# Kernel tuning notes

Measured on AMD Instinct MI355X. Metric: run time of the kernel, lower is better.

Reference implementation:

```python
import jax, jax.numpy as jnp
import numpy as np
import math

BN_EPS = 1e-5
L2_EPS = 1e-12
TEMPARATURE = 0.01
Q_IN_DIM = 256


def _masked_bn(y, mask, gamma, beta):
    # y: [S, L, D], mask: [S, L] float (1 = valid packed row).
    # Emulates BatchNorm1d (training mode) over the packed valid rows.
    m = mask[..., None]
    cnt = jnp.sum(mask)
    mean = jnp.sum(y * m, axis=(0, 1)) / cnt
    var = jnp.sum(jnp.square(y - mean) * m, axis=(0, 1)) / cnt  # biased var
    return (y - mean) * jax.lax.rsqrt(var + BN_EPS) * gamma + beta


def _ctx_proj(x, W, b, gamma, beta, mask, normalize):
    y = jnp.einsum('sld,od->slo', x, W) + b
    y = jax.nn.relu(_masked_bn(y, mask, gamma, beta))
    if normalize:
        n = jnp.linalg.norm(y, axis=-1, keepdims=True)
        y = y / jnp.maximum(n, L2_EPS)
    return y


def setup_inputs() -> dict:
    key = jax.random.key(0)
    ks = jax.random.split(key, 8)
    S, La, Lb = 256, 128, 512
    Dq, Dkv, Dqk, Dv = 256, 265, 512, 512
    A = jax.random.normal(ks[0], (S, La, Dq), jnp.float32)
    B = jax.random.normal(ks[1], (S, Lb, Dkv), jnp.float32)
    a_lens = jax.random.randint(ks[2], (S,), 1, La + 1, jnp.int32)
    b_lens = jax.random.randint(ks[3], (S,), 1, Lb + 1, jnp.int32)
    pk = jax.random.split(ks[4], 4)
    sc = 0.05
    return {
        'A': A, 'B': B, 'a_lens': a_lens, 'b_lens': b_lens,
        'Wq': sc * jax.random.normal(pk[0], (Dqk, Dq), jnp.float32),
        'bq': jnp.zeros((Dqk,), jnp.float32),
        'gq': jnp.ones((Dqk,), jnp.float32),
        'betaq': jnp.zeros((Dqk,), jnp.float32),
        'Wk': sc * jax.random.normal(pk[1], (Dqk, Dkv), jnp.float32),
        'bk': jnp.zeros((Dqk,), jnp.float32),
        'gk': jnp.ones((Dqk,), jnp.float32),
        'betak': jnp.zeros((Dqk,), jnp.float32),
        'Wv': sc * jax.random.normal(pk[2], (Dv, Dkv), jnp.float32),
        'bv': jnp.zeros((Dv,), jnp.float32),
        'gv': jnp.ones((Dv,), jnp.float32),
        'betav': jnp.zeros((Dv,), jnp.float32),
        'Wf': sc * jax.random.normal(pk[3], (Dq, Dv), jnp.float32),
        'bf': jnp.zeros((Dq,), jnp.float32),
        'gf': jnp.ones((Dq,), jnp.float32),
        'betaf': jnp.zeros((Dq,), jnp.float32),
    }


def reference(A, B, a_lens, b_lens,
              Wq, bq, gq, betaq,
              Wk, bk, gk, betak,
              Wv, bv, gv, betav,
              Wf, bf, gf, betaf):
    S, La, _ = A.shape
    Lb = B.shape[1]
    mask_a = (jnp.arange(La)[None, :] < a_lens[:, None]).astype(A.dtype)  # [S, La]
    mask_b = (jnp.arange(Lb)[None, :] < b_lens[:, None]).astype(B.dtype)  # [S, Lb]

    q = _ctx_proj(A, Wq, bq, gq, betaq, mask_a, True)   # [S, La, Dqk]
    k = _ctx_proj(B, Wk, bk, gk, betak, mask_b, True)   # [S, Lb, Dqk]
    v = _ctx_proj(B, Wv, bv, gv, betav, mask_b, True)   # [S, Lb, Dv]

    scaler = 1.0 / (TEMPARATURE * math.sqrt(Q_IN_DIM))
    scores = jnp.einsum('sad,sbd->sab', q, k) * scaler  # [S, La, Lb]
    scores = jnp.where(mask_b[:, None, :] > 0, scores, -1e30)
    w = jax.nn.softmax(scores, axis=-1)
    wv = jnp.einsum('sab,sbd->sad', w, v)               # [S, La, Dv]

    f = _ctx_proj(wv, Wf, bf, gf, betaf, mask_a, False)  # [S, La, Dq]
    return f * mask_a[..., None]
```

## Files before the change

### kernel.cpp

```cpp
#include <hip/hip_runtime.h>
#include <hip/hip_bf16.h>
#include <stdint.h>


typedef __attribute__((ext_vector_type(8))) short short8;
typedef __attribute__((ext_vector_type(4))) float floatx4;

__device__ __forceinline__ float bf2f(short h) {
    union { unsigned u; float f; } c;
    c.u = ((unsigned)(unsigned short)h) << 16;
    return c.f;
}
__device__ __forceinline__ short f2bf(float f) {
    union { float f; unsigned u; } c;
    c.f = f;
    unsigned u = c.u + 0x7fffu + ((c.u >> 16) & 1u);
    return (short)(u >> 16);
}

__device__ __forceinline__ void async_cp16(const short* g, short* l) {
    __builtin_amdgcn_global_load_lds(
        (const __attribute__((address_space(1))) unsigned int*)g,
        (__attribute__((address_space(3))) unsigned int*)l, 16, 0, 0);
}

__device__ __forceinline__ short8 cvt8load(const float* p) {
    float4 f0 = *(const float4*)(p);
    float4 f1 = *(const float4*)(p + 4);
    short8 r;
    r[0] = f2bf(f0.x); r[1] = f2bf(f0.y); r[2] = f2bf(f0.z); r[3] = f2bf(f0.w);
    r[4] = f2bf(f1.x); r[5] = f2bf(f1.y); r[6] = f2bf(f1.z); r[7] = f2bf(f1.w);
    return r;
}
__device__ __forceinline__ short8 cvt8guard(const float* row, int c0, int Kin) {
    short8 r;
#pragma unroll
    for (int j = 0; j < 8; j++) {
        int c = c0 + j;
        r[j] = (c < Kin) ? f2bf(row[c]) : (short)0;
    }
    return r;
}

__global__ __launch_bounds__(256) void cvt_pad(const float* __restrict__ in,
                                               short* __restrict__ out,
                                               int kin, int kout) {
    long row = blockIdx.x;
    const float* src = in + row * (long)kin;
    short* dst = out + row * (long)kout;
    for (int c = threadIdx.x; c < kout; c += 256)
        dst[c] = (c < kin) ? f2bf(src[c]) : (short)0;
}

__global__ __launch_bounds__(256, 2)
void gemm128x2(const short* __restrict__ X,
               const short* __restrict__ W0, const short* __restrict__ W1,
               const float* __restrict__ bias0, const float* __restrict__ bias1,
               short* __restrict__ Y0, short* __restrict__ Y1,
               float* __restrict__ st0, float* __restrict__ st1,
               int N, int Kp, const int* __restrict__ lens, int Lshift,
               int nShift)
{
    __shared__ short SH[36864];
    const int lin = blockIdx.x;
    const int xcd = lin & 7, sl = lin >> 3;
    const int nb = sl & ((1 << nShift) - 1);
    const int ms = sl >> nShift;
    const int m0 = (ms * 8 + xcd) * 128;
    const int n0 = nb * 128;

    const int tid = threadIdx.x;
    const int l = tid & 63, w = tid >> 6;
    const int quad = l >> 4, l15 = l & 15;
    const int wr = w & 1, wc = w >> 1;
    const int mo = wr * 64, no = wc * 64;

    floatx4 acc0[4][4], acc1[4][4];
#pragma unroll
    for (int i = 0; i < 4; i++)
#pragma unroll
        for (int j = 0; j < 4; j++) {
            acc0[i][j] = (floatx4){0.f, 0.f, 0.f, 0.f};
            acc1[i][j] = (floatx4){0.f, 0.f, 0.f, 0.f};
        }

    int srow[2], scolS[2];
#pragma unroll
    for (int c = 0; c < 2; c++) {
        int L = tid * 16 + c * 4096;
        int S = L ^ ((((L >> 6) ^ (L >> 8)) & 1) << 4)
                  ^ (((L >> 7) & 1) << 5)
                  ^ (((L >> 8) & 1) << 6);
        srow[c] = S >> 6;
        scolS[c] = (S & 48) >> 1;
    }
    const short* Xs[2];
    const short* W0s[2];
    const short* W1s[2];
#pragma unroll
    for (int c = 0; c < 2; c++) {
        Xs[c]  = X  + (long)(m0 + srow[c]) * Kp + scolS[c];
        W0s[c] = W0 + (long)(n0 + srow[c]) * Kp + scolS[c];
        W1s[c] = W1 + (long)(n0 + srow[c]) * Kp + scolS[c];
    }
    const int nsteps = Kp >> 5;

    int rsA[4], rsB[4];
#pragma unroll
    for (int i = 0; i < 4; i++) {
        int rA = mo + i * 16 + l15;
        int rB = no + i * 16 + l15;
        rsA[i] = (rA << 6) ^ ((rA & 7) << 4) ^ (quad << 4);
        rsB[i] = (rB << 6) ^ ((rB & 7) << 4) ^ (quad << 4);
    }

    auto stage = [&](int buf, int t) {
        short* At = SH + buf * 12288;
        short* B0t = At + 4096;
        short* B1t = At + 8192;
        const int ko = t * 32;
#pragma unroll
        for (int c = 0; c < 2; c++)
            async_cp16(Xs[c] + ko, At + c * 2048 + tid * 8);
#pragma unroll
        for (int c = 0; c < 2; c++)
            async_cp16(W0s[c] + ko, B0t + c * 2048 + tid * 8);
#pragma unroll
        for (int c = 0; c < 2; c++)
            async_cp16(W1s[c] + ko, B1t + c * 2048 + tid * 8);
    };

    stage(0, 0);
    if (nsteps > 1) stage(1, 1);
    if (nsteps > 2) stage(2, 2);

    int cur = 0;
    for (int t = 0; t < nsteps; t++) {
        if (t + 2 < nsteps)      asm volatile("s_waitcnt vmcnt(12)" ::: "memory");
        else if (t + 1 < nsteps) asm volatile("s_waitcnt vmcnt(6)" ::: "memory");
        else                     asm volatile("s_waitcnt vmcnt(0)" ::: "memory");
        __builtin_amdgcn_s_barrier();
        __builtin_amdgcn_sched_barrier(0);

        const char* At = (const char*)(SH + cur * 12288);
        const char* B0t = At + 8192;
        const char* B1t = At + 16384;
        short8 af[4], bfr[4];
#pragma unroll
        for (int i = 0; i < 4; i++)
            af[i] = *(const short8*)(At + rsA[i]);
#pragma unroll
        for (int j = 0; j < 4; j++)
            bfr[j] = *(const short8*)(B0t + rsB[j]);
#pragma unroll
        for (int i = 0; i < 4; i++)
#pragma unroll
            for (int j = 0; j < 4; j++)
                acc0[i][j] = __builtin_amdgcn_mfma_f32_16x16x32_bf16(af[i], bfr[j], acc0[i][j], 0, 0, 0);
#pragma unroll
        for (int j = 0; j < 4; j++)
            bfr[j] = *(const short8*)(B1t + rsB[j]);
#pragma unroll
        for (int i = 0; i < 4; i++)
#pragma unroll
            for (int j = 0; j < 4; j++)
                acc1[i][j] = __builtin_amdgcn_mfma_f32_16x16x32_bf16(af[i], bfr[j], acc1[i][j], 0, 0, 0);

        __builtin_amdgcn_sched_barrier(0);
        __builtin_amdgcn_s_barrier();
        if (t + 3 < nsteps) stage(cur, t + 3);
        cur = (cur == 2) ? 0 : cur + 1;
    }

    const int Lmask = (1 << Lshift) - 1;
    float msk[4][4];
#pragma unroll
    for (int i = 0; i < 4; i++)
#pragma unroll
        for (int r = 0; r < 4; r++) {
            int rg = m0 + mo + i * 16 + quad * 4 + r;
            msk[i][r] = ((rg & Lmask) < lens[rg >> Lshift]) ? 1.f : 0.f;
        }
    short* Cs = SH;

    auto epi = [&](floatx4 (&acc)[4][4], const float* bias, float* stats, short* Y) {
        float bv[4];
#pragma unroll
        for (int j = 0; j < 4; j++) bv[j] = bias[n0 + no + j * 16 + l15];
#pragma unroll
        for (int j = 0; j < 4; j++) {
            float ps = 0.f, pss = 0.f;
#pragma unroll
            for (int i = 0; i < 4; i++)
#pragma unroll
                for (int r = 0; r < 4; r++) {
                    float v = acc[i][j][r] + bv[j];
                    ps += v * msk[i][r];
                    pss += v * v * msk[i][r];
                }
            ps  += __shfl_xor(ps, 16, 64);  ps  += __shfl_xor(ps, 32, 64);
            pss += __shfl_xor(pss, 16, 64); pss += __shfl_xor(pss, 32, 64);
            if (l < 16) {
                atomicAdd(&stats[n0 + no + j * 16 + l15], ps);
                atomicAdd(&stats[N + n0 + no + j * 16 + l15], pss);
            }
        }
#pragma unroll
        for (int pass = 0; pass < 2; pass++) {
            __syncthreads();
            if (wr == pass) {
#pragma unroll
                for (int j = 0; j < 4; j++)
#pragma unroll
                    for (int i = 0; i < 4; i++)
#pragma unroll
                        for (int r = 0; r < 4; r++)
                            Cs[(i * 16 + quad * 4 + r) * 132 + no + j * 16 + l15] =
                                f2bf(acc[i][j][r] + bv[j]);
            }
            __syncthreads();
#pragma unroll
            for (int c = 0; c < 4; c++) {
                int e = c * 2048 + tid * 8;
                int row = e >> 7, col = e & 127;
                short8 vv = *(const short8*)(Cs + row * 132 + col);
                *(short8*)(Y + (long)(m0 + pass * 64 + row) * N + n0 + col) = vv;
            }
        }
    };
    epi(acc0, bias0, st0, Y0);
    epi(acc1, bias1, st1, Y1);
}

__global__ __launch_bounds__(256, 3)
void gemm128(const short* __restrict__ X,
             const short* __restrict__ W0, const short* __restrict__ W1,
             const float* __restrict__ bias0, const float* __restrict__ bias1,
             short* __restrict__ Y0, short* __restrict__ Y1,
             float* __restrict__ st0, float* __restrict__ st1,
             int N, int Kp, const int* __restrict__ lens, int Lshift,
             int nShift, int dual)
{
    __shared__ short SH[24576];
    const int lin = blockIdx.x;
    const int xcd = lin & 7, sl = lin >> 3;
    const int nb = sl & ((1 << nShift) - 1);
    const int ms = sl >> nShift;
    const int m0 = (ms * 8 + xcd) * 128;
    int g = 0, n0;
    if (dual) { g = nb & 1; n0 = (nb >> 1) * 128; } else { n0 = nb * 128; }
    const short* W    = g ? W1 : W0;
    const float* bias = g ? bias1 : bias0;
    short* Y          = g ? Y1 : Y0;
    float* stats      = g ? st1 : st0;

    const int tid = threadIdx.x;
    const int l = tid & 63, w = tid >> 6;
    const int quad = l >> 4, l15 = l & 15;
    const int wr = w & 1, wc = w >> 1;
    const int mo = wr * 64, no = wc * 64;

    floatx4 acc[4][4];
#pragma unroll
    for (int i = 0; i < 4; i++)
#pragma unroll
        for (int j = 0; j < 4; j++) acc[i][j] = (floatx4){0.f, 0.f, 0.f, 0.f};

    const int srow = tid >> 2;
    const int scol = (tid & 3) * 8;
    const short* Xs = X + (long)(m0 + srow) * Kp + scol;
    const short* Ws = W + (long)(n0 + srow) * Kp + scol;
    const long strideR = (long)64 * Kp;
    const int nsteps = Kp >> 5;

    auto stage = [&](int buf, int t) {
        short* At = SH + buf * 8192;
        short* Bt = At + 4096;
        const short* Xk = Xs + t * 32;
        const short* Wk = Ws + t * 32;
        async_cp16(Xk,           At + tid * 8);
        async_cp16(Xk + strideR, At + 2048 + tid * 8);
        async_cp16(Wk,           Bt + tid * 8);
        async_cp16(Wk + strideR, Bt + 2048 + tid * 8);
    };

    stage(0, 0);
    if (nsteps > 1) stage(1, 1);
    if (nsteps > 2) stage(2, 2);

    int cur = 0;
    for (int t = 0; t < nsteps; t++) {
        if (t + 2 < nsteps)      asm volatile("s_waitcnt vmcnt(8)" ::: "memory");
        else if (t + 1 < nsteps) asm volatile("s_waitcnt vmcnt(4)" ::: "memory");
        else                     asm volatile("s_waitcnt vmcnt(0)" ::: "memory");
        __builtin_amdgcn_s_barrier();
        __builtin_amdgcn_sched_barrier(0);

        const short* At = SH + cur * 8192;
        const short* Bt = At + 4096;
        short8 af[4], bfr[4];
#pragma unroll
        for (int i = 0; i < 4; i++)
            af[i] = *(const short8*)(At + (mo + i * 16 + l15) * 32 + quad * 8);
#pragma unroll
        for (int j = 0; j < 4; j++)
            bfr[j] = *(const short8*)(Bt + (no + j * 16 + l15) * 32 + quad * 8);
#pragma unroll
        for (int i = 0; i < 4; i++)
#pragma unroll
            for (int j = 0; j < 4; j++)
                acc[i][j] = __builtin_amdgcn_mfma_f32_16x16x32_bf16(af[i], bfr[j], acc[i][j], 0, 0, 0);

        __builtin_amdgcn_sched_barrier(0);
        __builtin_amdgcn_s_barrier();
        if (t + 3 < nsteps) stage(cur, t + 3);
        cur = (cur == 2) ? 0 : cur + 1;
    }

    const int Lmask = (1 << Lshift) - 1;
    float msk[4][4];
#pragma unroll
    for (int i = 0; i < 4; i++)
#pragma unroll
        for (int r = 0; r < 4; r++) {
            int rg = m0 + mo + i * 16 + quad * 4 + r;
            msk[i][r] = ((rg & Lmask) < lens[rg >> Lshift]) ? 1.f : 0.f;
        }
    float bv[4];
#pragma unroll
    for (int j = 0; j < 4; j++) bv[j] = bias[n0 + no + j * 16 + l15];

#pragma unroll
    for (int j = 0; j < 4; j++) {
        float ps = 0.f, pss = 0.f;
#pragma unroll
        for (int i = 0; i < 4; i++)
#pragma unroll
            for (int r = 0; r < 4; r++) {
                float v = acc[i][j][r] + bv[j];
                ps += v * msk[i][r];
                pss += v * v * msk[i][r];
            }
        ps  += __shfl_xor(ps, 16, 64);  ps  += __shfl_xor(ps, 32, 64);
        pss += __shfl_xor(pss, 16, 64); pss += __shfl_xor(pss, 32, 64);
        if (l < 16) {
            atomicAdd(&stats[n0 + no + j * 16 + l15], ps);
            atomicAdd(&stats[N + n0 + no + j * 16 + l15], pss);
        }
    }

    short* Cs = SH;
#pragma unroll
    for (int pass = 0; pass < 2; pass++) {
        __syncthreads();
        if (wr == pass) {
#pragma unroll
            for (int j = 0; j < 4; j++)
#pragma unroll
                for (int i = 0; i < 4; i++)
#pragma unroll
                    for (int r = 0; r < 4; r++)
                        Cs[(i * 16 + quad * 4 + r) * 132 + no + j * 16 + l15] =
                            f2bf(acc[i][j][r] + bv[j]);
        }
        __syncthreads();
#pragma unroll
        for (int c = 0; c < 4; c++) {
            int e = c * 2048 + tid * 8;
            int row = e >> 7, col = e & 127;
            short8 vv = *(const short8*)(Cs + row * 132 + col);
            *(short8*)(Y + (long)(m0 + pass * 64 + row) * N + n0 + col) = vv;
        }
    }
}

template<bool XBF16, bool KAL>
__global__ __launch_bounds__(256, 2)
void gemm_bt(const void* __restrict__ Xp, const float* __restrict__ W,
             const float* __restrict__ bias, short* __restrict__ Y,
             int N, int Kin, int Kp, float* __restrict__ stats,
             const int* __restrict__ lens, int Lshift)
{
    __shared__ short At[128 * 32];
    __shared__ short Bt[128 * 32];
    const int m0 = blockIdx.x * 128;
    const int n0 = blockIdx.y * 128;
    const int tid = threadIdx.x;
    const int w = tid >> 6, l = tid & 63;
    const int quad = l >> 4, l15 = l & 15;
    const int mo = (w & 1) * 64, no = (w >> 1) * 64;

    floatx4 acc[4][4];
#pragma unroll
    for (int i = 0; i < 4; i++)
#pragma unroll
        for (int j = 0; j < 4; j++) acc[i][j] = (floatx4){0.f, 0.f, 0.f, 0.f};

    const int srow = tid >> 2;
    const int sc8 = (tid & 3) * 8;

    for (int k0 = 0; k0 < Kp; k0 += 32) {
        __syncthreads();
        const int c0 = k0 + sc8;
        short8 a0, a1, b0, b1;
        if (XBF16) {
            const short* X = (const short*)Xp;
            a0 = *(const short8*)(X + (long)(m0 + srow) * Kp + c0);
            a1 = *(const short8*)(X + (long)(m0 + 64 + srow) * Kp + c0);
        } else {
            const float* X = (const float*)Xp;
            if (KAL) {
                a0 = cvt8load(X + (long)(m0 + srow) * Kin + c0);
                a1 = cvt8load(X + (long)(m0 + 64 + srow) * Kin + c0);
            } else {
                a0 = cvt8guard(X + (long)(m0 + srow) * Kin, c0, Kin);
                a1 = cvt8guard(X + (long)(m0 + 64 + srow) * Kin, c0, Kin);
            }
        }
        if (KAL) {
            b0 = cvt8load(W + (long)(n0 + srow) * Kin + c0);
            b1 = cvt8load(W + (long)(n0 + 64 + srow) * Kin + c0);
        } else {
            b0 = cvt8guard(W + (long)(n0 + srow) * Kin, c0, Kin);
            b1 = cvt8guard(W + (long)(n0 + 64 + srow) * Kin, c0, Kin);
        }
        *(short8*)(At + srow * 32 + sc8) = a0;
        *(short8*)(At + (64 + srow) * 32 + sc8) = a1;
        *(short8*)(Bt + srow * 32 + sc8) = b0;
        *(short8*)(Bt + (64 + srow) * 32 + sc8) = b1;
        __syncthreads();
        short8 af[4], bfr[4];
#pragma unroll
        for (int i = 0; i < 4; i++) {
            af[i]  = *(const short8*)(At + (mo + i * 16 + l15) * 32 + quad * 8);
            bfr[i] = *(const short8*)(Bt + (no + i * 16 + l15) * 32 + quad * 8);
        }
#pragma unroll
        for (int i = 0; i < 4; i++)
#pragma unroll
            for (int j = 0; j < 4; j++)
                acc[i][j] = __builtin_amdgcn_mfma_f32_16x16x32_bf16(af[i], bfr[j], acc[i][j], 0, 0, 0);
    }

    const int Lmask = (1 << Lshift) - 1;
    float msk[4][4];
#pragma unroll
    for (int i = 0; i < 4; i++)
#pragma unroll
        for (int r = 0; r < 4; r++) {
            int rg = m0 + mo + i * 16 + quad * 4 + r;
            msk[i][r] = ((rg & Lmask) < lens[rg >> Lshift]) ? 1.f : 0.f;
        }
#pragma unroll
    for (int j = 0; j < 4; j++) {
        int colj = n0 + no + j * 16 + l15;
        float bvs = bias[colj];
        float ps = 0.f, pss = 0.f;
#pragma unroll
        for (int i = 0; i < 4; i++)
#pragma unroll
            for (int r = 0; r < 4; r++) {
                int rg = m0 + mo + i * 16 + quad * 4 + r;
                float v = acc[i][j][r] + bvs;
                Y[(long)rg * N + colj] = f2bf(v);
                ps += v * msk[i][r];
                pss += v * v * msk[i][r];
            }
        ps  += __shfl_xor(ps, 16, 64);  ps  += __shfl_xor(ps, 32, 64);
        pss += __shfl_xor(pss, 16, 64); pss += __shfl_xor(pss, 32, 64);
        if (l < 16) {
            atomicAdd(&stats[colj], ps);
            atomicAdd(&stats[N + colj], pss);
        }
    }
}

__global__ void finalize_stats(float* __restrict__ stats, const float* __restrict__ g,
                               const float* __restrict__ beta,
                               const int* __restrict__ lens, int C)
{
    __shared__ int lred[256];
    int t = threadIdx.x;
    if (t < 256) lred[t] = lens[t];
    __syncthreads();
    for (int s2 = 128; s2 > 0; s2 >>= 1) {
        if (t < s2) lred[t] += lred[t + s2];
        __syncthreads();
    }
    float cnt = (float)lred[0];
    if (t < C) {
        float mean = stats[t] / cnt;
        float var = fmaxf(stats[C + t] / cnt - mean * mean, 0.f);
        float a = rsqrtf(var + 1e-5f) * g[t];
        stats[t] = a;
        stats[C + t] = beta[t] - mean * a;
    }
}

__global__ __launch_bounds__(256)
void apply_norm512(short* __restrict__ Y, const float* __restrict__ stats)
{
    int w = threadIdx.x >> 6, l = threadIdx.x & 63;
    long row = (long)blockIdx.x * 4 + w;
    short8 yv = *(const short8*)(Y + row * 512 + l * 8);
    float v[8];
    float ss = 0.f;
#pragma unroll
    for (int i = 0; i < 8; i++) {
        int c = l * 8 + i;
        float t = fmaxf(bf2f(yv[i]) * stats[c] + stats[512 + c], 0.f);
        v[i] = t;
        ss += t * t;
    }
#pragma unroll
    for (int off = 1; off < 64; off <<= 1) ss += __shfl_xor(ss, off, 64);
    float scl = 1.f / fmaxf(sqrtf(ss), 1e-12f);
    short8 o;
#pragma unroll
    for (int i = 0; i < 8; i++) o[i] = f2bf(v[i] * scl);
    *(short8*)(Y + row * 512 + l * 8) = o;
}

__global__ __launch_bounds__(256)
void attention(const short* __restrict__ q, const short* __restrict__ k,
               const short* __restrict__ v, const int* __restrict__ b_lens,
               short* __restrict__ wv, int wvStride)
{
    __shared__ short tile[32 * 520];
    __shared__ short Pscr[4][16 * 40];
    const int lin = blockIdx.x;
    const int xcd = lin & 7, sl = lin >> 3;
    const int a0 = (sl & 1) * 64;
    const int s = (sl >> 1) * 8 + xcd;
    const int tid = threadIdx.x;
    const int w = tid >> 6, l = tid & 63;
    const int quad = l >> 4, l15 = l & 15;
    const int blen = b_lens[s];
    const int sr = tid >> 3;
    const int scg = (tid & 7) * 8;

    short8 qf[16];
    const short* qbase = q + ((long)(s * 128 + a0 + w * 16 + l15)) * 512 + quad * 8;
#pragma unroll
    for (int kk = 0; kk < 16; kk++) qf[kk] = *(const short8*)(qbase + kk * 32);

    floatx4 sc[32];
#pragma unroll
    for (int i = 0; i < 32; i++) sc[i] = (floatx4){0.f, 0.f, 0.f, 0.f};

    const short* kbase = k + (long)s * 512 * 512;
    for (int bt2 = 0; bt2 < 16; ++bt2) {
        __syncthreads();
        const short* krow = kbase + (long)(bt2 * 32 + sr) * 512;
#pragma unroll
        for (int i = 0; i < 2; i++) {
            short8 t0 = *(const short8*)(krow + i * 256 + scg);
            short8 t1 = *(const short8*)(krow + i * 256 + 64 + scg);
            short8 t2 = *(const short8*)(krow + i * 256 + 128 + scg);
            short8 t3 = *(const short8*)(krow + i * 256 + 192 + scg);
            *(short8*)(&tile[sr * 520 + i * 256 + scg]) = t0;
            *(short8*)(&tile[sr * 520 + i * 256 + 64 + scg]) = t1;
            *(short8*)(&tile[sr * 520 + i * 256 + 128 + scg]) = t2;
            *(short8*)(&tile[sr * 520 + i * 256 + 192 + scg]) = t3;
        }
        __syncthreads();
#pragma unroll
        for (int kk = 0; kk < 16; kk++) {
            short8 f0 = *(const short8*)(&tile[l15 * 520 + kk * 32 + quad * 8]);
            short8 f1 = *(const short8*)(&tile[(16 + l15) * 520 + kk * 32 + quad * 8]);
            sc[bt2 * 2]     = __builtin_amdgcn_mfma_f32_16x16x32_bf16(qf[kk], f0, sc[bt2 * 2], 0, 0, 0);
            sc[bt2 * 2 + 1] = __builtin_amdgcn_mfma_f32_16x16x32_bf16(qf[kk], f1, sc[bt2 * 2 + 1], 0, 0, 0);
        }
    }

    const float scaler = 6.25f;
    float mrow[4] = {-__builtin_inff(), -__builtin_inff(), -__builtin_inff(), -__builtin_inff()};
#pragma unroll
    for (int bt = 0; bt < 32; ++bt) {
        bool valid = (bt * 16 + l15) < blen;
#pragma unroll
        for (int r = 0; r < 4; r++) {
            float v2 = valid ? sc[bt][r] * scaler : -__builtin_inff();
            sc[bt][r] = v2;
            mrow[r] = fmaxf(mrow[r], v2);
        }
    }
#pragma unroll
    for (int r = 0; r < 4; r++) {
#pragma unroll
        for (int off = 1; off < 16; off <<= 1)
            mrow[r] = fmaxf(mrow[r], __shfl_xor(mrow[r], off, 64));
    }
    float ssum[4] = {0.f, 0.f, 0.f, 0.f};
#pragma unroll
    for (int bt = 0; bt < 32; ++bt)
#pragma unroll
        for (int r = 0; r < 4; r++) {
            float p = __expf(sc[bt][r] - mrow[r]);
            sc[bt][r] = p;
            ssum[r] += p;
        }
#pragma unroll
    for (int r = 0; r < 4; r++) {
#pragma unroll
        for (int off = 1; off < 16; off <<= 1) ssum[r] += __shfl_xor(ssum[r], off, 64);
        ssum[r] = 1.f / ssum[r];
    }

    short8 pf[16];
    short* Pw = Pscr[w];
#pragma unroll
    for (int kk = 0; kk < 16; kk++) {
#pragma unroll
        for (int half = 0; half < 2; half++)
#pragma unroll
            for (int r = 0; r < 4; r++)
                Pw[(quad * 4 + r) * 40 + half * 16 + l15] = f2bf(sc[kk * 2 + half][r] * ssum[r]);
        pf[kk] = *(const short8*)(&Pw[l15 * 40 + quad * 8]);
    }

    const short* vbase = v + (long)s * 512 * 512;
    short* wvbase = wv + (long)(s * 128 + a0 + w * 16 + quad * 4) * wvStride;
    for (int dt = 0; dt < 16; ++dt) {
        __syncthreads();
#pragma unroll
        for (int round = 0; round < 2; round++) {
            int b = round * 256 + tid;
            const short* vr = vbase + (long)b * 512 + dt * 32;
            short8 x0 = *(const short8*)(vr);
            short8 x1 = *(const short8*)(vr + 8);
            short8 x2 = *(const short8*)(vr + 16);
            short8 x3 = *(const short8*)(vr + 24);
#pragma unroll
            for (int j = 0; j < 8; j++) {
                tile[j * 520 + b]        = x0[j];
                tile[(8 + j) * 520 + b]  = x1[j];
                tile[(16 + j) * 520 + b] = x2[j];
                tile[(24 + j) * 520 + b] = x3[j];
            }
        }
        __syncthreads();
        floatx4 o0 = (floatx4){0.f, 0.f, 0.f, 0.f};
        floatx4 o1 = (floatx4){0.f, 0.f, 0.f, 0.f};
#pragma unroll
        for (int kk = 0; kk < 16; kk++) {
            short8 f0 = *(const short8*)(&tile[l15 * 520 + kk * 32 + quad * 8]);
            short8 f1 = *(const short8*)(&tile[(16 + l15) * 520 + kk * 32 + quad * 8]);
            o0 = __builtin_amdgcn_mfma_f32_16x16x32_bf16(pf[kk], f0, o0, 0, 0, 0);
            o1 = __builtin_amdgcn_mfma_f32_16x16x32_bf16(pf[kk], f1, o1, 0, 0, 0);
        }
#pragma unroll
        for (int r = 0; r < 4; r++) {
            wvbase[(long)r * wvStride + dt * 32 + l15]      = f2bf(o0[r]);
            wvbase[(long)r * wvStride + dt * 32 + 16 + l15] = f2bf(o1[r]);
        }
    }

    if (wvStride > 512) {
        int r = tid >> 2, cb = (tid & 3) * 16;
        short8 z = (short8){0, 0, 0, 0, 0, 0, 0, 0};
        short* pz = wv + (long)(s * 128 + a0 + r) * wvStride + 512 + cb;
        *(short8*)(pz) = z;
        *(short8*)(pz + 8) = z;
    }
}

__global__ __launch_bounds__(256)
void apply_f(const short* __restrict__ Yf, const float* __restrict__ stats,
             const int* __restrict__ a_lens, float* __restrict__ out)
{
    const long total = (long)32768 * 256;
    for (long e = (long)blockIdx.x * 256 + threadIdx.x; e < total; e += (long)gridDim.x * 256) {
        int c = (int)(e & 255);
        long row = e >> 8;
        int sI = (int)(row >> 7), pos = (int)(row & 127);
        float v = fmaxf(bf2f(Yf[e]) * stats[c] + stats[256 + c], 0.f);
        out[e] = (pos < a_lens[sI]) ? v : 0.f;
    }
}

extern "C" void kernel_launch(void* const* d_in, const int* in_sizes, int n_in,
                              void* d_out, int out_size, void* d_ws, size_t ws_size,
                              hipStream_t stream)
{
    (void)in_sizes; (void)n_in; (void)out_size;
    const float* A     = (const float*)d_in[0];
    const float* B     = (const float*)d_in[1];
    const int* a_lens  = (const int*)d_in[2];
    const int* b_lens  = (const int*)d_in[3];
    const float* Wq    = (const float*)d_in[4];
    const float* bq    = (const float*)d_in[5];
    const float* gq    = (const float*)d_in[6];
    const float* betaq = (const float*)d_in[7];
    const float* Wk    = (const float*)d_in[8];
    const float* bk    = (const float*)d_in[9];
    const float* gk    = (const float*)d_in[10];
    const float* betak = (const float*)d_in[11];
    const float* Wv    = (const float*)d_in[12];
    const float* bv    = (const float*)d_in[13];
    const float* gv    = (const float*)d_in[14];
    const float* betav = (const float*)d_in[15];
    const float* Wf    = (const float*)d_in[16];
    const float* bfp   = (const float*)d_in[17];
    const float* gf    = (const float*)d_in[18];
    const float* betaf = (const float*)d_in[19];
    float* out = (float*)d_out;
    char* base = (char*)d_ws;

    const size_t oWqb = 0;
    const size_t oWkb = oWqb + 294912;
    const size_t oWvb = oWkb + 294912;
    const size_t oWfb = oWvb + 294912;
    const size_t oBbf = oWfb + 294912;
    const size_t oQb  = oBbf + 75497472;
    const size_t oYv  = oQb + 33554432;
    const size_t oKb  = oYv + 134217728;
    const size_t oSt  = oKb + 134217728;
    const size_t FAST_NEED = oSt + 16384;

    if (ws_size >= FAST_NEED) {
        short* Wqb = (short*)(base + oWqb);
        short* Wkb = (short*)(base + oWkb);
        short* Wvb = (short*)(base + oWvb);
        short* Wfb = (short*)(base + oWfb);
        short* Bbf = (short*)(base + oBbf);
        short* qb  = (short*)(base + oQb);
        short* Yv  = (short*)(base + oYv);
        short* kb  = (short*)(base + oKb);
        short* Abf = (short*)(base + oKb);
        short* wvb = (short*)(base + oBbf);
        short* Yf  = (short*)(base + oQb);
        float* stQ = (float*)(base + oSt);
        float* stK = stQ + 1024;
        float* stV = stQ + 2048;
        float* stF = stQ + 3072;

        hipMemsetAsync(stQ, 0, 16384, stream);

        cvt_pad<<<32768, 256, 0, stream>>>(A, Abf, 256, 288);
        cvt_pad<<<131072, 256, 0, stream>>>(B, Bbf, 265, 288);
        cvt_pad<<<512, 256, 0, stream>>>(Wq, Wqb, 256, 288);
        cvt_pad<<<512, 256, 0, stream>>>(Wk, Wkb, 265, 288);
        cvt_pad<<<512, 256, 0, stream>>>(Wv, Wvb, 265, 288);
        cvt_pad<<<256, 256, 0, stream>>>(Wf, Wfb, 512, 576);

        gemm128<<<1024, 256, 0, stream>>>(
            Abf, Wqb, Wqb, bq, bq, qb, qb, stQ, stQ, 512, 288, a_lens, 7, 2, 0);
        gemm128x2<<<4096, 256, 0, stream>>>(
            Bbf, Wvb, Wkb, bv, bk, Yv, kb, stV, stK, 512, 288, b_lens, 9, 2);

        finalize_stats<<<1, 512, 0, stream>>>(stV, gv, betav, b_lens, 512);
        finalize_stats<<<1, 512, 0, stream>>>(stK, gk, betak, b_lens, 512);
        finalize_stats<<<1, 512, 0, stream>>>(stQ, gq, betaq, a_lens, 512);
        apply_norm512<<<32768, 256, 0, stream>>>(Yv, stV);
        apply_norm512<<<32768, 256, 0, stream>>>(kb, stK);
        apply_norm512<<<8192, 256, 0, stream>>>(qb, stQ);

        attention<<<512, 256, 0, stream>>>(qb, kb, Yv, b_lens, wvb, 576);

        gemm128<<<512, 256, 0, stream>>>(
            wvb, Wfb, Wfb, bfp, bfp, Yf, Yf, stF, stF, 256, 576, a_lens, 7, 1, 0);
        finalize_stats<<<1, 512, 0, stream>>>(stF, gf, betaf, a_lens, 256);
        apply_f<<<8192, 256, 0, stream>>>(Yf, stF, a_lens, out);
        return;
    }

    short* qb  = (short*)(base);
    short* Yv  = (short*)(base + 33554432);
    short* kb  = (short*)(base + 33554432 + 134217728);
    short* wvb = (short*)(base + 33554432 + 2L * 134217728);
    float* stQ = (float*)(base + 2L * 33554432 + 2L * 134217728);
    float* stK = stQ + 1024;
    float* stV = stQ + 2048;
    float* stF = stQ + 3072;
    short* Yf  = qb;

    hipMemsetAsync(stQ, 0, 16384, stream);

    gemm_bt<false, true><<<dim3(256, 4), 256, 0, stream>>>(
        A, Wq, bq, qb, 512, 256, 256, stQ, a_lens, 7);
    gemm_bt<false, false><<<dim3(1024, 4), 256, 0, stream>>>(
        B, Wv, bv, Yv, 512, 265, 288, stV, b_lens, 9);
    finalize_stats<<<1, 512, 0, stream>>>(stV, gv, betav, b_lens, 512);
    apply_norm512<<<32768, 256, 0, stream>>>(Yv, stV);
    gemm_bt<false, false><<<dim3(1024, 4), 256, 0, stream>>>(
        B, Wk, bk, kb, 512, 265, 288, stK, b_lens, 9);
    finalize_stats<<<1, 512, 0, stream>>>(stK, gk, betak, b_lens, 512);
    apply_norm512<<<32768, 256, 0, stream>>>(kb, stK);
    finalize_stats<<<1, 512, 0, stream>>>(stQ, gq, betaq, a_lens, 512);
    apply_norm512<<<8192, 256, 0, stream>>>(qb, stQ);
    attention<<<512, 256, 0, stream>>>(qb, kb, Yv, b_lens, wvb, 512);
    gemm_bt<true, true><<<dim3(256, 2), 256, 0, stream>>>(
        wvb, Wf, bfp, Yf, 256, 512, 512, stF, a_lens, 7);
    finalize_stats<<<1, 512, 0, stream>>>(stF, gf, betaf, a_lens, 256);
    apply_f<<<8192, 256, 0, stream>>>(Yf, stF, a_lens, out);
}
```

Before: 837.5 us.

## Skip padded rows across conversion, projection GEMMs, normalization and attention

Uses a_lens and b_lens to skip work on padded sequence positions in several stages. The B conversion, the fused K/V projection GEMM tiles, the K/V normalization blocks and the attention key loop now exit early or stop at the valid length rounded up to the tile size. Attention blocks whose query rows are all padding just write zeros. This cuts memory traffic and MFMA work that only produced masked-out values, in exchange for per-block length checks and runtime (non-unrolled) loop bounds in attention, which may hurt register allocation for the pf/sc arrays.

```diff
diff --git a/kernel.cpp b/kernel.cpp
--- a/kernel.cpp
+++ b/kernel.cpp
@@ -46,6 +46,19 @@
                                                short* __restrict__ out,
                                                int kin, int kout) {
     long row = blockIdx.x;
+    const float* src = in + row * (long)kin;
+    short* dst = out + row * (long)kout;
+    for (int c = threadIdx.x; c < kout; c += 256)
+        dst[c] = (c < kin) ? f2bf(src[c]) : (short)0;
+}
+
+__global__ __launch_bounds__(256) void cvt_padB(const float* __restrict__ in,
+                                                short* __restrict__ out,
+                                                int kin, int kout,
+                                                const int* __restrict__ lens) {
+    long row = blockIdx.x;
+    int pos = (int)(row & 511), s = (int)(row >> 9);
+    if (pos >= ((lens[s] + 127) & ~127)) return;
     const float* src = in + row * (long)kin;
     short* dst = out + row * (long)kout;
     for (int c = threadIdx.x; c < kout; c += 256)
@@ -67,6 +80,7 @@
     const int nb = sl & ((1 << nShift) - 1);
     const int ms = sl >> nShift;
     const int m0 = (ms * 8 + xcd) * 128;
+    if ((m0 & ((1 << Lshift) - 1)) >= lens[m0 >> Lshift]) return;
     const int n0 = nb * 128;
 
     const int tid = threadIdx.x;
@@ -522,8 +536,36 @@
 }
 
 __global__ __launch_bounds__(256)
+void apply_norm512_len(short* __restrict__ Y, const float* __restrict__ stats,
+                       const int* __restrict__ lens)
+{
+    int bid = blockIdx.x;
+    if (((bid & 127) * 4) >= lens[bid >> 7]) return;
+    int w = threadIdx.x >> 6, l = threadIdx.x & 63;
+    long row = (long)bid * 4 + w;
+    short8 yv = *(const short8*)(Y + row * 512 + l * 8);
+    float v[8];
+    float ss = 0.f;
+#pragma unroll
+    for (int i = 0; i < 8; i++) {
+        int c = l * 8 + i;
+        float t = fmaxf(bf2f(yv[i]) * stats[c] + stats[512 + c], 0.f);
+        v[i] = t;
+        ss += t * t;
+    }
+#pragma unroll
+    for (int off = 1; off < 64; off <<= 1) ss += __shfl_xor(ss, off, 64);
+    float scl = 1.f / fmaxf(sqrtf(ss), 1e-12f);
+    short8 o;
+#pragma unroll
+    for (int i = 0; i < 8; i++) o[i] = f2bf(v[i] * scl);
+    *(short8*)(Y + row * 512 + l * 8) = o;
+}
+
+__global__ __launch_bounds__(256)
 void attention(const short* __restrict__ q, const short* __restrict__ k,
                const short* __restrict__ v, const int* __restrict__ b_lens,
+               const int* __restrict__ a_lens,
                short* __restrict__ wv, int wvStride)
 {
     __shared__ short tile[32 * 520];
@@ -536,6 +578,17 @@
     const int w = tid >> 6, l = tid & 63;
     const int quad = l >> 4, l15 = l & 15;
     const int blen = b_lens[s];
+
+    if (a_lens[s] <= a0) {
+        short8 z = (short8){0, 0, 0, 0, 0, 0, 0, 0};
+        short* wz = wv + (long)(s * 128 + a0) * wvStride;
+        const int total = 64 * wvStride;
+        for (int e = tid * 8; e < total; e += 2048)
+            *(short8*)(wz + e) = z;
+        return;
+    }
+
+    const int nkt = (blen + 31) >> 5;
     const int sr = tid >> 3;
     const int scg = (tid & 7) * 8;
 
@@ -549,7 +602,7 @@
     for (int i = 0; i < 32; i++) sc[i] = (floatx4){0.f, 0.f, 0.f, 0.f};
 
     const short* kbase = k + (long)s * 512 * 512;
-    for (int bt2 = 0; bt2 < 16; ++bt2) {
+    for (int bt2 = 0; bt2 < nkt; ++bt2) {
         __syncthreads();
         const short* krow = kbase + (long)(bt2 * 32 + sr) * 512;
 #pragma unroll
@@ -609,8 +662,7 @@
 
     short8 pf[16];
     short* Pw = Pscr[w];
-#pragma unroll
-    for (int kk = 0; kk < 16; kk++) {
+    for (int kk = 0; kk < nkt; kk++) {
 #pragma unroll
         for (int half = 0; half < 2; half++)
 #pragma unroll
@@ -619,6 +671,7 @@
         pf[kk] = *(const short8*)(&Pw[l15 * 40 + quad * 8]);
     }
 
+    const int nb32 = nkt * 32;
     const short* vbase = v + (long)s * 512 * 512;
     short* wvbase = wv + (long)(s * 128 + a0 + w * 16 + quad * 4) * wvStride;
     for (int dt = 0; dt < 16; ++dt) {
@@ -626,24 +679,25 @@
 #pragma unroll
         for (int round = 0; round < 2; round++) {
             int b = round * 256 + tid;
-            const short* vr = vbase + (long)b * 512 + dt * 32;
-            short8 x0 = *(const short8*)(vr);
-            short8 x1 = *(const short8*)(vr + 8);
-            short8 x2 = *(const short8*)(vr + 16);
-            short8 x3 = *(const short8*)(vr + 24);
-#pragma unroll
-            for (int j = 0; j < 8; j++) {
-                tile[j * 520 + b]        = x0[j];
-                tile[(8 + j) * 520 + b]  = x1[j];
-                tile[(16 + j) * 520 + b] = x2[j];
-                tile[(24 + j) * 520 + b] = x3[j];
+            if (b < nb32) {
+                const short* vr = vbase + (long)b * 512 + dt * 32;
+                short8 x0 = *(const short8*)(vr);
+                short8 x1 = *(const short8*)(vr + 8);
+                short8 x2 = *(const short8*)(vr + 16);
+                short8 x3 = *(const short8*)(vr + 24);
+#pragma unroll
+                for (int j = 0; j < 8; j++) {
+                    tile[j * 520 + b]        = x0[j];
+                    tile[(8 + j) * 520 + b]  = x1[j];
+                    tile[(16 + j) * 520 + b] = x2[j];
+                    tile[(24 + j) * 520 + b] = x3[j];
+                }
             }
         }
         __syncthreads();
         floatx4 o0 = (floatx4){0.f, 0.f, 0.f, 0.f};
         floatx4 o1 = (floatx4){0.f, 0.f, 0.f, 0.f};
-#pragma unroll
-        for (int kk = 0; kk < 16; kk++) {
+        for (int kk = 0; kk < nkt; kk++) {
             short8 f0 = *(const short8*)(&tile[l15 * 520 + kk * 32 + quad * 8]);
             short8 f1 = *(const short8*)(&tile[(16 + l15) * 520 + kk * 32 + quad * 8]);
             o0 = __builtin_amdgcn_mfma_f32_16x16x32_bf16(pf[kk], f0, o0, 0, 0, 0);
@@ -738,7 +792,7 @@
         hipMemsetAsync(stQ, 0, 16384, stream);
 
         cvt_pad<<<32768, 256, 0, stream>>>(A, Abf, 256, 288);
-        cvt_pad<<<131072, 256, 0, stream>>>(B, Bbf, 265, 288);
+        cvt_padB<<<131072, 256, 0, stream>>>(B, Bbf, 265, 288, b_lens);
         cvt_pad<<<512, 256, 0, stream>>>(Wq, Wqb, 256, 288);
         cvt_pad<<<512, 256, 0, stream>>>(Wk, Wkb, 265, 288);
         cvt_pad<<<512, 256, 0, stream>>>(Wv, Wvb, 265, 288);
@@ -752,11 +806,11 @@
         finalize_stats<<<1, 512, 0, stream>>>(stV, gv, betav, b_lens, 512);
         finalize_stats<<<1, 512, 0, stream>>>(stK, gk, betak, b_lens, 512);
         finalize_stats<<<1, 512, 0, stream>>>(stQ, gq, betaq, a_lens, 512);
-        apply_norm512<<<32768, 256, 0, stream>>>(Yv, stV);
-        apply_norm512<<<32768, 256, 0, stream>>>(kb, stK);
+        apply_norm512_len<<<32768, 256, 0, stream>>>(Yv, stV, b_lens);
+        apply_norm512_len<<<32768, 256, 0, stream>>>(kb, stK, b_lens);
         apply_norm512<<<8192, 256, 0, stream>>>(qb, stQ);
 
-        attention<<<512, 256, 0, stream>>>(qb, kb, Yv, b_lens, wvb, 576);
+        attention<<<512, 256, 0, stream>>>(qb, kb, Yv, b_lens, a_lens, wvb, 576);
 
         gemm128<<<512, 256, 0, stream>>>(
             wvb, Wfb, Wfb, bfp, bfp, Yf, Yf, stF, stF, 256, 576, a_lens, 7, 1, 0);
@@ -789,7 +843,7 @@
     apply_norm512<<<32768, 256, 0, stream>>>(kb, stK);
     finalize_stats<<<1, 512, 0, stream>>>(stQ, gq, betaq, a_lens, 512);
     apply_norm512<<<8192, 256, 0, stream>>>(qb, stQ);
-    attention<<<512, 256, 0, stream>>>(qb, kb, Yv, b_lens, wvb, 512);
+    attention<<<512, 256, 0, stream>>>(qb, kb, Yv, b_lens, a_lens, wvb, 512);
     gemm_bt<true, true><<<dim3(256, 2), 256, 0, stream>>>(
         wvb, Wf, bfp, Yf, 256, 512, 512, stF, a_lens, 7);
     finalize_stats<<<1, 512, 0, stream>>>(stF, gf, betaf, a_lens, 256);
```

Result: faster. 817.4 us (-2.4%).
